# Optimization experiments

Hardware: AMD Instinct MI355X
Metric: run time of the kernel (lower is better)

The kernel has to match this reference:

```python
import jax, jax.numpy as jnp
import numpy as np

HIDDEN = 128; HEADS = 8; HD = HIDDEN // HEADS; NRBF = 50; NLAYERS = 6
CUT = 5.0; MAXZ = 100
N = 5000; E = 100000


def cosine_cutoff(d):
    # cutoff_lower = 0: 0.5*(cos(pi*d/cut)+1) * (d < cut)
    return 0.5 * (jnp.cos(d * (jnp.pi / CUT)) + 1.0) * (d < CUT)


def expnorm_rbf(d, means, betas):
    # ExpNormalSmearing with cutoff_lower=0, alpha = 5/cutoff
    alpha = 5.0 / CUT
    return cosine_cutoff(d)[:, None] * jnp.exp(-betas * (jnp.exp(-alpha * d)[:, None] - means) ** 2)


def layernorm(x, w, b):
    m = x.mean(-1, keepdims=True)
    v = ((x - m) ** 2).mean(-1, keepdims=True)
    return (x - m) / jnp.sqrt(v + 1e-5) * w + b


def setup_inputs():
    key = jax.random.key(0)
    ks = jax.random.split(key, 16)
    start = float(np.exp(-CUT))

    def lin(k, fi, fo):
        return jax.random.normal(k, (fi, fo), jnp.float32) / np.sqrt(fi)

    def lin_l(k, fi, fo):
        return jax.random.normal(k, (NLAYERS, fi, fo), jnp.float32) / np.sqrt(fi)

    return {
        "z": jax.random.randint(ks[0], (N,), 0, MAXZ),
        "edge_index": jax.random.randint(ks[1], (2, E), 0, N),
        "edge_vec": jax.random.normal(ks[2], (E, 3), jnp.float32) * 1.7,
        "emb": jax.random.normal(ks[3], (MAXZ, HIDDEN), jnp.float32),
        "means": jnp.linspace(start, 1.0, NRBF, dtype=jnp.float32),
        "betas": jnp.full((NRBF,), (2.0 / NRBF * (1.0 - start)) ** -2, dtype=jnp.float32),
        "ne_emb": jax.random.normal(ks[4], (MAXZ, HIDDEN), jnp.float32),
        "dpW": lin(ks[5], NRBF, HIDDEN), "dpb": jnp.zeros((HIDDEN,), jnp.float32),
        "cbW": lin(ks[6], 2 * HIDDEN, HIDDEN), "cbb": jnp.zeros((HIDDEN,), jnp.float32),
        "lnw": jnp.ones((NLAYERS, HIDDEN), jnp.float32), "lnb": jnp.zeros((NLAYERS, HIDDEN), jnp.float32),
        "qW": lin_l(ks[7], HIDDEN, HIDDEN), "qb": jnp.zeros((NLAYERS, HIDDEN), jnp.float32),
        "kW": lin_l(ks[8], HIDDEN, HIDDEN), "kb": jnp.zeros((NLAYERS, HIDDEN), jnp.float32),
        "vW": lin_l(ks[9], HIDDEN, 3 * HIDDEN), "vb": jnp.zeros((NLAYERS, 3 * HIDDEN), jnp.float32),
        "oW": lin_l(ks[10], HIDDEN, 3 * HIDDEN), "ob": jnp.zeros((NLAYERS, 3 * HIDDEN), jnp.float32),
        "vecW": lin_l(ks[11], HIDDEN, 3 * HIDDEN),
        "dkW": lin_l(ks[12], NRBF, HIDDEN), "dkb": jnp.zeros((NLAYERS, HIDDEN), jnp.float32),
        "dvW": lin_l(ks[13], NRBF, 3 * HIDDEN), "dvb": jnp.zeros((NLAYERS, 3 * HIDDEN), jnp.float32),
        "onw": jnp.ones((HIDDEN,), jnp.float32), "onb": jnp.zeros((HIDDEN,), jnp.float32),
    }


def _forward(z, edge_index, edge_vec, emb, means, betas, ne_emb, dpW, dpb, cbW, cbb,
             lnw, lnb, qW, qb, kW, kb, vW, vb, oW, ob, vecW, dkW, dkb, dvW, dvb, onw, onb):
    src, dst = edge_index[0], edge_index[1]          # j (source), i (target)
    n = z.shape[0]
    x = emb[z]                                        # [N, H]
    ew = jnp.linalg.norm(edge_vec, axis=1)            # [E]
    ea = expnorm_rbf(ew, means, betas)                # [E, NRBF]
    nonself = src != dst
    # normalize edge vectors except self-loop edges (kept as-is, matching the torch clone/mask)
    evn = edge_vec / jnp.where(nonself, ew, 1.0)[:, None]
    cut_e = cosine_cutoff(ew)                         # [E]

    # --- NeighborEmbedding: self-loops removed from aggregation ---
    W = (ea @ dpW + dpb) * cut_e[:, None]
    W = jnp.where(nonself[:, None], W, 0.0)
    agg = jax.ops.segment_sum(ne_emb[z][src] * W, dst, num_segments=n)
    x = jnp.concatenate([x, agg], axis=1) @ cbW + cbb
    vec = jnp.zeros((n, 3, HIDDEN), x.dtype)

    def layer(carry, p):
        x, vec = carry
        h = layernorm(x, p["lnw"], p["lnb"])
        q = (h @ p["qW"] + p["qb"]).reshape(n, HEADS, HD)
        k = (h @ p["kW"] + p["kb"]).reshape(n, HEADS, HD)
        v = (h @ p["vW"] + p["vb"]).reshape(n, HEADS, 3 * HD)
        vec1, vec2, vec3 = jnp.split(jnp.einsum("nch,hk->nck", vec, p["vecW"]), 3, axis=-1)
        vec_dot = (vec1 * vec2).sum(axis=1)                    # [N, H]
        vec_h = vec.reshape(n, 3, HEADS, HD)
        dk = jax.nn.silu(ea @ p["dkW"] + p["dkb"]).reshape(-1, HEADS, HD)
        dv = jax.nn.silu(ea @ p["dvW"] + p["dvb"]).reshape(-1, HEADS, 3 * HD)
        # per-edge attention weight, silu activation, smoothly cut off
        attn = jax.nn.silu((q[dst] * k[src] * dk).sum(-1)) * cut_e[:, None]   # [E, heads]
        xm, w1, w2 = jnp.split(v[src] * dv, 3, axis=2)                        # each [E, heads, HD]
        xm = xm * attn[:, :, None]
        vecm = vec_h[src] * w1[:, None] + w2[:, None] * evn[:, :, None, None] # [E, 3, heads, HD]
        xa = jax.ops.segment_sum(xm, dst, num_segments=n).reshape(n, HIDDEN)
        va = jax.ops.segment_sum(vecm, dst, num_segments=n).reshape(n, 3, HIDDEN)
        o1, o2, o3 = jnp.split(xa @ p["oW"] + p["ob"], 3, axis=-1)
        dx = vec_dot * o2 + o3
        dvec = vec3 * o1[:, None, :] + va
        return (x + dx, vec + dvec), None

    stacked = {"lnw": lnw, "lnb": lnb, "qW": qW, "qb": qb, "kW": kW, "kb": kb,
               "vW": vW, "vb": vb, "oW": oW, "ob": ob, "vecW": vecW,
               "dkW": dkW, "dkb": dkb, "dvW": dvW, "dvb": dvb}
    (x, vec), _ = jax.lax.scan(layer, (x, vec), stacked)
    x = layernorm(x, onw, onb)
    return x, vec


def reference(z, edge_index, edge_vec, emb, means, betas, ne_emb, dpW, dpb, cbW, cbb,
              lnw, lnb, qW, qb, kW, kb, vW, vb, oW, ob, vecW, dkW, dkb, dvW, dvb, onw, onb):
    return _forward(z, edge_index, edge_vec, emb, means, betas, ne_emb, dpW, dpb, cbW, cbb,
                    lnw, lnb, qW, qb, kW, kb, vW, vb, oW, ob, vecW, dkW, dkb, dvW, dvb, onw, onb)
```

## Files before the change

### kernel.cpp

```cpp
#include <hip/hip_runtime.h>
#include <math.h>

#define HID 128
#define NRBF 50
#define NLAYERS 6
#define CUTV 5.0f
#define KNOTS 1024
#define TSCALE 204.8f
#define TINV   0.0048828125f
#define TROWS  (KNOTS + 1)
#define TRWORDS 512
#define TSTRIDE ((size_t)TROWS * TRWORDS)
#define WCOLS 1408
#define KB 16

typedef unsigned int  uint32;
typedef unsigned short ushort16;
typedef __attribute__((ext_vector_type(8))) short short8;
typedef __attribute__((ext_vector_type(4))) float f32x4;

__device__ __forceinline__ float siluf(float x){ return x / (1.0f + __expf(-x)); }
__device__ __forceinline__ float lerpf(float a, float b, float f){ return fmaf(f, b - a, a); }
__device__ __forceinline__ ushort16 f2b(float x){
    uint32 u = __float_as_uint(x);
    u += 0x7fffu + ((u >> 16) & 1u);
    return (ushort16)(u >> 16);
}
__device__ __forceinline__ float b2f(ushort16 u){ return __uint_as_float(((uint32)u) << 16); }
__device__ __forceinline__ uint32 packp(float a, float b){
    return (uint32)f2b(a) | ((uint32)f2b(b) << 16);
}
__device__ __forceinline__ float plo(uint32 u){ return __uint_as_float(u << 16); }
__device__ __forceinline__ float phi(uint32 u){ return __uint_as_float(u & 0xffff0000u); }
__device__ __forceinline__ float plerp(uint32 u, float f){ float a = plo(u); return fmaf(f, phi(u) - a, a); }

__global__ void k_count(const int* ei, int E, int* counts){
    int e = blockIdx.x*blockDim.x + threadIdx.x;
    if (e < E) atomicAdd(&counts[ei[E + e]], 1);
}

__global__ void k_scan(const int* counts, int* offsets, int* cursor, int n){
    __shared__ int part[1024];
    int tid = threadIdx.x;
    int PER = (n + 1023) >> 10;
    int base = tid * PER;
    int loc[8]; int s = 0;
    #pragma unroll 8
    for (int ii = 0; ii < 8; ii++){
        if (ii < PER){
            int idx = base + ii;
            int c = (idx < n) ? counts[idx] : 0;
            loc[ii] = s; s += c;
        }
    }
    part[tid] = s;
    __syncthreads();
    for (int off = 1; off < 1024; off <<= 1){
        int v = (tid >= off) ? part[tid - off] : 0;
        __syncthreads();
        part[tid] += v;
        __syncthreads();
    }
    int excl = (tid == 0) ? 0 : part[tid - 1];
    #pragma unroll 8
    for (int ii = 0; ii < 8; ii++){
        if (ii < PER){
            int idx = base + ii;
            if (idx < n){ int o = excl + loc[ii]; offsets[idx] = o; cursor[idx] = o; }
        }
    }
    if (tid == 1023) offsets[n] = part[1023];
}

__global__ void k_scatter(const int* ei, int E, int* cursor, int* eperm){
    int e = blockIdx.x*blockDim.x + threadIdx.x;
    if (e < E){
        int d = ei[E + e];
        int pos = atomicAdd(&cursor[d], 1);
        eperm[pos] = e;
    }
}

__global__ __launch_bounds__(256) void k_srcsort(const int* offsets, const int* ei, int* eperm, int N){
    int node = blockIdx.x*4 + (threadIdx.x >> 6);
    int lane = threadIdx.x & 63;
    if (node >= N) return;
    int r0 = offsets[node], r1 = offsets[node+1];
    for (int c0 = r0; c0 < r1; c0 += 64){
        int n = min(64, r1 - c0);
        int e = 0; int key = 0x7fffffff;
        if (lane < n){ e = eperm[c0 + lane]; key = ei[e]; }
        int rank = 0;
        for (int t = 0; t < n; t++){
            int kt = __shfl(key, t, 64);
            if (t != lane && ((kt < key) || (kt == key && t < lane))) rank++;
        }
        if (lane < n) eperm[c0 + rank] = e;
    }
}

__global__ void k_edge_vals(const int* ei, const float* edge_vec, const int* eperm, int E,
                            int4* edata, float4* evn4){
    int row = blockIdx.x*blockDim.x + threadIdx.x;
    if (row >= E) return;
    int e = eperm[row];
    int s = ei[e], d = ei[E + e];
    float vx = edge_vec[e*3+0], vy = edge_vec[e*3+1], vz = edge_vec[e*3+2];
    float ew = sqrtf(vx*vx + vy*vy + vz*vz);
    float cut = (ew < CUTV) ? 0.5f*(__cosf(ew * 0.62831853071795864f) + 1.0f) : 0.0f;
    int ns = (s != d) ? 1 : 0;
    float inv = ns ? (1.0f/ew) : 1.0f;
    float un = fminf(ew * TSCALE, (float)KNOTS);
    int j = (int)un;
    float f = un - (float)j;
    int4 ed; ed.x = s; ed.y = j; ed.z = __float_as_int(f); ed.w = __float_as_int(cut);
    edata[row] = ed;
    float4 ev; ev.x = vx*inv; ev.y = vy*inv; ev.z = vz*inv; ev.w = ns ? 1.0f : 0.0f;
    evn4[row] = ev;
}

__global__ void k_pad(ushort16* hb16, ushort16* vecm, ushort16* xab16, int N, int Nup, int N3up){
    int i = blockIdx.x*blockDim.x + threadIdx.x;
    int hpad = (Nup - N)*HID;
    int vpad = (N3up - 3*N)*HID;
    if (i < hpad){ hb16[(size_t)N*HID + i] = 0; xab16[(size_t)N*HID + i] = 0; }
    if (i < vpad) vecm[(size_t)3*N*HID + i] = 0;
}

__global__ void k_prep_nemb(const int* z, const float* ne_emb, ushort16* nemb16, int total){
    int idx = blockIdx.x*256 + threadIdx.x;
    if (idx >= total) return;
    int n = idx >> 7, h = idx & 127;
    nemb16[idx] = f2b(ne_emb[(size_t)z[n]*HID + h]);
}

__global__ __launch_bounds__(512) void k_build_tables(
    const float* means, const float* betas,
    const float* dkW, const float* dkb, const float* dvW, const float* dvb,
    uint32* Tp){
    int jb = blockIdx.x * KB;
    int l  = blockIdx.y;
    int c  = threadIdx.x;
    __shared__ float ea_s[KB+1][NRBF+2];
    for (int idx = c; idx < (KB+1)*NRBF; idx += 512){
        int kk = idx / NRBF, r = idx - kk*NRBF;
        float d = (jb + kk) * TINV;
        float cut = (d < CUTV) ? 0.5f*(__cosf(d * 0.62831853071795864f) + 1.0f) : 0.0f;
        float u = __expf(-d) - means[r];
        ea_s[kk][r] = cut * __expf(-betas[r]*u*u);
    }
    __syncthreads();
    int h = c >> 2, i = c & 3;
    const float* Wcol; int stride; float bias;
    if (i == 0){
        Wcol = dkW + (size_t)l*NRBF*HID + h; stride = HID;
        bias = dkb[(size_t)l*HID + h];
    } else {
        int col = ((h >> 4)*48 + (h & 15)) + 16*(i-1);
        Wcol = dvW + (size_t)l*NRBF*384 + col; stride = 384;
        bias = dvb[(size_t)l*384 + col];
    }
    float a[KB+1];
    #pragma unroll
    for (int k = 0; k <= KB; k++) a[k] = bias;
    for (int r = 0; r < NRBF; r++){
        float w = Wcol[(size_t)r*stride];
        #pragma unroll
        for (int k = 0; k <= KB; k++) a[k] += ea_s[k][r]*w;
    }
    uint32* dst = Tp + (size_t)l*TSTRIDE + (size_t)jb*TRWORDS + c;
    float sp = siluf(a[0]);
    #pragma unroll
    for (int k = 0; k < KB; k++){
        int j = jb + k;
        if (j >= TROWS) break;
        float sn = siluf(a[k+1]);
        dst[(size_t)k*TRWORDS] = packp(sp, sn);
        sp = sn;
    }
}

__global__ __launch_bounds__(128) void k_build_ne(
    const float* means, const float* betas,
    const float* dpW, const float* dpb, uint32* Tne32){
    int j = blockIdx.x, c = threadIdx.x;
    __shared__ float ea0[NRBF], ea1[NRBF];
    float d0 = j * TINV, d1 = (j+1) * TINV;
    float c0 = (d0 < CUTV) ? 0.5f*(__cosf(d0 * 0.62831853071795864f) + 1.0f) : 0.0f;
    float c1 = (d1 < CUTV) ? 0.5f*(__cosf(d1 * 0.62831853071795864f) + 1.0f) : 0.0f;
    if (c < NRBF){
        float m = means[c], be = betas[c];
        float u0 = __expf(-d0) - m, u1 = __expf(-d1) - m;
        ea0[c] = c0 * __expf(-be*u0*u0);
        ea1[c] = c1 * __expf(-be*u1*u1);
    }
    __syncthreads();
    float a0 = dpb[c], a1 = a0;
    #pragma unroll
    for (int r = 0; r < NRBF; r++){ float w = dpW[r*HID + c]; a0 += ea0[r]*w; a1 += ea1[r]*w; }
    Tne32[(size_t)j*HID + c] = packp(a0*c0, a1*c1);
}

__global__ __launch_bounds__(256) void k_build_wt(
    const float* qW, const float* kW, const float* vW, const float* vecW, const float* oW,
    ushort16* WT){
    int l = blockIdx.y; int c0 = blockIdx.x*32;
    __shared__ ushort16 t[128][33];
    for (int i = threadIdx.x; i < 128*32; i += 256){
        int k = i >> 5, c = i & 31;
        int gcol = c0 + c;
        const float* W; int C; int oc;
        if (gcol < 128)      { W = qW   + (size_t)l*HID*128; C = 128; oc = gcol; }
        else if (gcol < 640) {
            int s = gcol - 128; int h = s >> 2, si = s & 3;
            if (si == 3){ W = kW + (size_t)l*HID*128; C = 128; oc = h; }
            else        { W = vW + (size_t)l*HID*384; C = 384; oc = (h>>4)*48 + (h&15) + 16*si; }
        }
        else if (gcol < 1024){ W = vecW + (size_t)l*HID*384; C = 384; oc = gcol-640; }
        else                 { W = oW   + (size_t)l*HID*384; C = 384; oc = gcol-1024; }
        t[k][c] = f2b(W[(size_t)k*C + oc]);
    }
    __syncthreads();
    ushort16* dst = WT + (size_t)l*WCOLS*HID + (size_t)c0*HID;
    for (int i = threadIdx.x; i < 128*32; i += 256){
        int c = i >> 7, k = i & 127;
        dst[(size_t)c*HID + k] = t[k][c];
    }
}

__global__ __launch_bounds__(512) void k_build_bias(
    const float* kb, const float* vb, float* kvbias){
    int l = blockIdx.x, s = threadIdx.x;
    int h = s >> 2, i = s & 3;
    float v = (i == 3) ? kb[(size_t)l*HID + h]
                       : vb[(size_t)l*384 + (h>>4)*48 + (h&15) + 16*i];
    kvbias[(size_t)l*512 + s] = v;
}

__global__ __launch_bounds__(256) void k_mfma01(
    const ushort16* __restrict__ hb16, const ushort16* __restrict__ vecm,
    const ushort16* __restrict__ WT, const float* __restrict__ qbias,
    const float* __restrict__ kvbias,
    float* __restrict__ qo, ushort16* __restrict__ vpack,
    ushort16* __restrict__ vecout, int N){
    int NT1 = (N + 63) >> 6;
    int NT3 = (3*N + 63) >> 6;
    int b = blockIdx.x;
    int cg, rblk;
    if (b < 10*NT1){ cg = b / NT1; rblk = (b - cg*NT1)*64; }
    else { int b2 = b - 10*NT1; int c2 = b2 / NT3; cg = 10 + c2; rblk = (b2 - c2*NT3)*64; }
    const ushort16* A; int R; int cblk; const ushort16* wt;
    if (cg < 10){ A = hb16; R = N;   cblk = cg*64;      wt = WT; }
    else        { A = vecm; R = 3*N; cblk = (cg-10)*64; wt = WT + (size_t)640*HID; }
    int wave = threadIdx.x >> 6, lane = threadIdx.x & 63;
    int r0 = rblk + wave*16;
    int l16 = lane & 15, lg = lane >> 4;
    short8 a[4];
    const ushort16* ar = A + (size_t)(r0 + l16)*HID + lg*8;
    #pragma unroll
    for (int ks = 0; ks < 4; ks++) a[ks] = *(const short8*)(ar + ks*32);
    f32x4 acc[4];
    #pragma unroll
    for (int ct = 0; ct < 4; ct++){ acc[ct][0]=0.f; acc[ct][1]=0.f; acc[ct][2]=0.f; acc[ct][3]=0.f; }
    #pragma unroll
    for (int ct = 0; ct < 4; ct++){
        const ushort16* br = wt + (size_t)(cblk + ct*16 + l16)*HID + lg*8;
        #pragma unroll
        for (int ks = 0; ks < 4; ks++){
            short8 bfr = *(const short8*)(br + ks*32);
            acc[ct] = __builtin_amdgcn_mfma_f32_16x16x32_bf16(a[ks], bfr, acc[ct], 0, 0, 0);
        }
    }
    __shared__ ushort16 lds[64][72];
    if (cg < 2){
        #pragma unroll
        for (int ct = 0; ct < 4; ct++){
            int gc = cblk + ct*16 + l16;
            float bb = qbias[gc];
            #pragma unroll
            for (int rg = 0; rg < 4; rg++){
                int row = r0 + lg*4 + rg;
                if (row < R) qo[(size_t)row*HID + gc] = acc[ct][rg] + bb;
            }
        }
        return;
    }
    const float* bias = (cg < 10) ? (kvbias + (cblk - 128)) : nullptr;
    #pragma unroll
    for (int ct = 0; ct < 4; ct++){
        int lc = ct*16 + l16;
        float bb = bias ? bias[lc] : 0.f;
        #pragma unroll
        for (int rg = 0; rg < 4; rg++)
            lds[wave*16 + lg*4 + rg][lc] = f2b(acc[ct][rg] + bb);
    }
    __syncthreads();
    ushort16* out; int stride, colbase;
    if (cg < 10){ out = vpack;  stride = 512; colbase = cblk - 128; }
    else        { out = vecout; stride = 384; colbase = cblk; }
    const uint32* l32 = (const uint32*)&lds[0][0];
    #pragma unroll
    for (int it = 0; it < 8; it++){
        int idx = it*256 + threadIdx.x;
        int row = idx >> 5, cp = idx & 31;
        int grow = rblk + row;
        if (grow < R){
            uint32 val = l32[row*36 + cp];
            *((uint32*)(out + (size_t)grow*stride + colbase) + cp) = val;
        }
    }
}

__global__ __launch_bounds__(128) void k_ne_agg(
    const int* __restrict__ offsets, const int4* __restrict__ edata,
    const uint32* __restrict__ Tne32, const ushort16* __restrict__ nemb16,
    float* __restrict__ agg){
    int i = blockIdx.x, h = threadIdx.x;
    float acc = 0.f;
    int r0 = offsets[i], r1 = offsets[i+1];
    for (int t0 = r0; t0 < r1; t0 += 4){
        uint32 tn_[4]; ushort16 nb_[4]; float f_[4]; int s_[4];
        #pragma unroll
        for (int u = 0; u < 4; u++){
            int row = min(t0 + u, r1 - 1);
            int4 ed = edata[row];
            s_[u] = ed.x;
            f_[u] = __int_as_float(ed.z);
            tn_[u] = Tne32[(size_t)ed.y*HID + h];
            nb_[u] = nemb16[(size_t)ed.x*HID + h];
        }
        #pragma unroll
        for (int u = 0; u < 4; u++){
            if (t0 + u >= r1) break;
            if (s_[u] != i) acc += plerp(tn_[u], f_[u]) * b2f(nb_[u]);
        }
    }
    agg[(size_t)i*HID + h] = acc;
}

__global__ __launch_bounds__(128) void k_combine_ln(
    const int* z, const float* emb, const float* agg, const float* cbW, const float* cbb,
    const float* lnw0, const float* lnb0,
    float* x, ushort16* hb16, float* vec, ushort16* vecm, uint32* vecpack, int N){
    int n0 = blockIdx.x*8, h = threadIdx.x;
    __shared__ float in_s[8][2*HID];
    int nr = min(8, N - n0);
    for (int m = 0; m < nr; m++){
        in_s[m][h]       = emb[(size_t)z[n0+m]*HID + h];
        in_s[m][HID + h] = agg[(size_t)(n0+m)*HID + h];
    }
    __syncthreads();
    float acc[8];
    #pragma unroll
    for (int m = 0; m < 8; m++) acc[m] = 0.f;
    for (int kk = 0; kk < 2*HID; kk += 4){
        float w0 = cbW[(kk+0)*HID + h], w1 = cbW[(kk+1)*HID + h];
        float w2 = cbW[(kk+2)*HID + h], w3 = cbW[(kk+3)*HID + h];
        #pragma unroll
        for (int m = 0; m < 8; m++){
            const float* a = &in_s[m][kk];
            acc[m] += a[0]*w0 + a[1]*w1 + a[2]*w2 + a[3]*w3;
        }
    }
    float bias = cbb[h], w = lnw0[h], bb = lnb0[h];
    __shared__ float r1_[2], r2_[2];
    int wid = h >> 6;
    for (int m = 0; m < nr; m++){
        int n = n0 + m;
        float v = acc[m] + bias;
        x[(size_t)n*HID + h] = v;
        float s1 = v, s2 = v*v;
        #pragma unroll
        for (int o = 32; o; o >>= 1){ s1 += __shfl_xor(s1, o, 64); s2 += __shfl_xor(s2, o, 64); }
        if ((h & 63) == 0){ r1_[wid] = s1; r2_[wid] = s2; }
        __syncthreads();
        float sum = r1_[0] + r1_[1], sumsq = r2_[0] + r2_[1];
        float mean = sum * (1.f/HID);
        float var = sumsq * (1.f/HID) - mean*mean;
        float inv = rsqrtf(var + 1e-5f);
        hb16[(size_t)n*HID + h] = f2b((v - mean)*inv*w + bb);
        __syncthreads();
        vec [(size_t)n*384 + h]       = 0.f;
        vec [(size_t)n*384 + 128 + h] = 0.f;
        vec [(size_t)n*384 + 256 + h] = 0.f;
        vecm[(size_t)n*384 + h]       = 0;
        vecm[(size_t)n*384 + 128 + h] = 0;
        vecm[(size_t)n*384 + 256 + h] = 0;
        vecpack[(size_t)n*256 + 2*h]     = 0;
        vecpack[(size_t)n*256 + 2*h + 1] = 0;
    }
}

__global__ __launch_bounds__(128) void k_edge_agg(
    const int* __restrict__ offsets, const int4* __restrict__ edata,
    const float4* __restrict__ evn4, const uint32* __restrict__ Tp,
    const float* __restrict__ q, const ushort16* __restrict__ vpack,
    const uint32* __restrict__ vecpack,
    ushort16* __restrict__ xa16, float* __restrict__ va){
    int i = blockIdx.x, h = threadIdx.x;
    float qv = q[(size_t)i*HID + h];
    float axa = 0.f, av0 = 0.f, av1 = 0.f, av2 = 0.f;
    int r0 = offsets[i], r1 = offsets[i+1];
    for (int t0 = r0; t0 < r1; t0 += 4){
        float f_[4], cut_[4], ex_[4], ey_[4], ez_[4];
        uint4 t4_[4];
        uint2 vp_[4], vc_[4];
        #pragma unroll
        for (int u = 0; u < 4; u++){
            int row = min(t0 + u, r1 - 1);
            int4 ed = edata[row];
            int s = ed.x, j = ed.y;
            f_[u]   = __int_as_float(ed.z);
            cut_[u] = __int_as_float(ed.w);
            t4_[u] = *(const uint4*)(Tp + (size_t)j*TRWORDS + 4*h);
            vp_[u] = *(const uint2*)((const uint32*)(vpack + (size_t)s*512) + 2*h);
            vc_[u] = *(const uint2*)(vecpack + (size_t)s*256 + 2*h);
            float4 ev = evn4[row];
            ex_[u] = ev.x; ey_[u] = ev.y; ez_[u] = ev.z;
        }
        #pragma unroll
        for (int u = 0; u < 4; u++){
            if (t0 + u >= r1) break;
            float f = f_[u];
            float dk = plerp(t4_[u].x, f);
            float kv = phi(vp_[u].y);
            float p = qv * kv * dk;
            p += __shfl_xor(p, 1, 64);
            p += __shfl_xor(p, 2, 64);
            p += __shfl_xor(p, 4, 64);
            p += __shfl_xor(p, 8, 64);
            float attn = siluf(p) * cut_[u];
            float dv0 = plerp(t4_[u].y, f);
            float dv1 = plerp(t4_[u].z, f);
            float dv2 = plerp(t4_[u].w, f);
            axa += plo(vp_[u].x) * dv0 * attn;
            float w1v = phi(vp_[u].x) * dv1;
            float w2v = plo(vp_[u].y) * dv2;
            av0 += plo(vc_[u].x)*w1v + w2v*ex_[u];
            av1 += phi(vc_[u].x)*w1v + w2v*ey_[u];
            av2 += plo(vc_[u].y)*w1v + w2v*ez_[u];
        }
    }
    xa16[(size_t)i*HID + h] = f2b(axa);
    va[(size_t)i*384 + h]       = av0;
    va[(size_t)i*384 + 128 + h] = av1;
    va[(size_t)i*384 + 256 + h] = av2;
}

#define OROWS 32
__global__ __launch_bounds__(256) void k_oupd(
    const ushort16* __restrict__ xab16, const ushort16* __restrict__ WT,
    const float* __restrict__ obias,
    float* __restrict__ x, float* __restrict__ vec, ushort16* __restrict__ vecm,
    uint32* __restrict__ vecpack,
    const ushort16* __restrict__ vecout, const float* __restrict__ va,
    const float* __restrict__ lnw_n, const float* __restrict__ lnb_n,
    ushort16* __restrict__ hb16, float* __restrict__ outx, float* __restrict__ outv,
    int N, int fin){
    __shared__ float o_s[OROWS][385];
    int tile = blockIdx.x; int r0 = tile*OROWS;
    int wid = threadIdx.x >> 6, lane = threadIdx.x & 63;
    int l16 = lane & 15, lg = lane >> 4;
    {
        int rr = r0 + (wid & 1)*16;
        const ushort16* ar = xab16 + (size_t)(rr + l16)*HID + lg*8;
        short8 a[4];
        #pragma unroll
        for (int ks = 0; ks < 4; ks++) a[ks] = *(const short8*)(ar + ks*32);
        int cbase = (wid >> 1)*192;
        const ushort16* wt = WT + (size_t)1024*HID;
        #pragma unroll
        for (int ct = 0; ct < 12; ct++){
            f32x4 acc; acc[0]=0.f; acc[1]=0.f; acc[2]=0.f; acc[3]=0.f;
            const ushort16* br = wt + (size_t)(cbase + ct*16 + l16)*HID + lg*8;
            #pragma unroll
            for (int ks = 0; ks < 4; ks++){
                short8 b = *(const short8*)(br + ks*32);
                acc = __builtin_amdgcn_mfma_f32_16x16x32_bf16(a[ks], b, acc, 0, 0, 0);
            }
            int gc = cbase + ct*16 + l16;
            float bb = obias[gc];
            #pragma unroll
            for (int rg = 0; rg < 4; rg++)
                o_s[(wid & 1)*16 + lg*4 + rg][gc] = acc[rg] + bb;
        }
    }
    __syncthreads();
    for (int pass = 0; pass < 8; pass++){
        int nrow = pass*4 + wid;
        int n = r0 + nrow;
        if (n >= N) break;
        const ushort16* vo = vecout + (size_t)n*1152;
        const float* o_r = o_s[nrow];
        size_t vb = (size_t)n*384;
        float xva, xvb, v0a, v0b, v1a, v1b, v2a, v2b;
        #pragma unroll
        for (int half = 0; half < 2; half++){
            int hh = lane + half*64;
            float vdot = b2f(vo[hh])*b2f(vo[128+hh]) + b2f(vo[384+hh])*b2f(vo[512+hh])
                       + b2f(vo[768+hh])*b2f(vo[896+hh]);
            float o1 = o_r[hh], o2 = o_r[128+hh], o3 = o_r[256+hh];
            float xv = x[(size_t)n*HID + hh] + vdot*o2 + o3;
            float v0 = vec[vb + hh]       + b2f(vo[256  + hh])*o1 + va[vb + hh];
            float v1 = vec[vb + 128 + hh] + b2f(vo[640  + hh])*o1 + va[vb + 128 + hh];
            float v2 = vec[vb + 256 + hh] + b2f(vo[1024 + hh])*o1 + va[vb + 256 + hh];
            if (half == 0){ xva = xv; v0a = v0; v1a = v1; v2a = v2; }
            else          { xvb = xv; v0b = v0; v1b = v1; v2b = v2; }
        }
        float s1 = xva + xvb, s2 = xva*xva + xvb*xvb;
        #pragma unroll
        for (int o = 32; o; o >>= 1){ s1 += __shfl_xor(s1, o, 64); s2 += __shfl_xor(s2, o, 64); }
        float mean = s1 * (1.f/HID);
        float var = s2 * (1.f/HID) - mean*mean;
        float inv = rsqrtf(var + 1e-5f);
        #pragma unroll
        for (int half = 0; half < 2; half++){
            int hh = lane + half*64;
            float xv = half ? xvb : xva;
            float v0 = half ? v0b : v0a;
            float v1 = half ? v1b : v1a;
            float v2 = half ? v2b : v2a;
            float lnv = (xv - mean)*inv*lnw_n[hh] + lnb_n[hh];
            if (!fin){
                x[(size_t)n*HID + hh] = xv;
                vec[vb + hh] = v0; vec[vb + 128 + hh] = v1; vec[vb + 256 + hh] = v2;
                vecm[vb + hh] = f2b(v0); vecm[vb + 128 + hh] = f2b(v1); vecm[vb + 256 + hh] = f2b(v2);
                vecpack[(size_t)n*256 + 2*hh]     = packp(v0, v1);
                vecpack[(size_t)n*256 + 2*hh + 1] = packp(v2, 0.f);
                hb16[(size_t)n*HID + hh] = f2b(lnv);
            } else {
                outx[(size_t)n*HID + hh] = lnv;
                outv[vb + hh] = v0; outv[vb + 128 + hh] = v1; outv[vb + 256 + hh] = v2;
            }
        }
    }
}

extern "C" void kernel_launch(void* const* d_in, const int* in_sizes, int n_in,
                              void* d_out, int out_size, void* d_ws, size_t ws_size,
                              hipStream_t stream){
    const int*   z        = (const int*)  d_in[0];
    const int*   ei       = (const int*)  d_in[1];
    const float* edge_vec = (const float*)d_in[2];
    const float* emb      = (const float*)d_in[3];
    const float* means    = (const float*)d_in[4];
    const float* betas    = (const float*)d_in[5];
    const float* ne_emb   = (const float*)d_in[6];
    const float* dpW      = (const float*)d_in[7];
    const float* dpb      = (const float*)d_in[8];
    const float* cbW      = (const float*)d_in[9];
    const float* cbb      = (const float*)d_in[10];
    const float* lnw      = (const float*)d_in[11];
    const float* lnb      = (const float*)d_in[12];
    const float* qW       = (const float*)d_in[13];
    const float* qb       = (const float*)d_in[14];
    const float* kW       = (const float*)d_in[15];
    const float* kb       = (const float*)d_in[16];
    const float* vW       = (const float*)d_in[17];
    const float* vb       = (const float*)d_in[18];
    const float* oW       = (const float*)d_in[19];
    const float* obias    = (const float*)d_in[20];
    const float* vecW     = (const float*)d_in[21];
    const float* dkW      = (const float*)d_in[22];
    const float* dkb      = (const float*)d_in[23];
    const float* dvW      = (const float*)d_in[24];
    const float* dvb      = (const float*)d_in[25];
    const float* onw      = (const float*)d_in[26];
    const float* onb      = (const float*)d_in[27];

    int N = in_sizes[0];
    int E = in_sizes[1] / 2;
    int Nup  = ((N + 63) >> 6) << 6;
    int N3up = ((3*N + 63) >> 6) << 6;

    char* p = (char*)d_ws;
    auto alloc = [&](size_t bytes){ void* r = (void*)p; p += (bytes + 255) & ~(size_t)255; return r; };
    int*      counts  = (int*)     alloc((size_t)N*4);
    int*      offsets = (int*)     alloc((size_t)(N+1)*4);
    int*      cursor  = (int*)     alloc((size_t)N*4);
    int*      eperm   = (int*)     alloc((size_t)E*4);
    int4*     edata   = (int4*)    alloc((size_t)E*16);
    float4*   evn4    = (float4*)  alloc((size_t)E*16);
    uint32*   Tp      = (uint32*)  alloc((size_t)NLAYERS*TSTRIDE*4);
    uint32*   Tne32   = (uint32*)  alloc((size_t)TROWS*HID*4);
    ushort16* WT      = (ushort16*)alloc((size_t)NLAYERS*WCOLS*HID*2);
    float*    kvbias  = (float*)   alloc((size_t)NLAYERS*512*4);
    ushort16* nemb16  = (ushort16*)alloc((size_t)N*HID*2);
    float*    agg     = (float*)   alloc((size_t)N*HID*4);
    float*    xb      = (float*)   alloc((size_t)N*HID*4);
    ushort16* hb16    = (ushort16*)alloc((size_t)Nup*HID*2);
    float*    qb_     = (float*)   alloc((size_t)N*HID*4);
    ushort16* vpack   = (ushort16*)alloc((size_t)N*512*2);
    uint32*   vecpack = (uint32*)  alloc((size_t)N*256*4);
    ushort16* vecm    = (ushort16*)alloc((size_t)N3up*HID*2);
    float*    vecb    = (float*)   alloc((size_t)N*384*4);
    ushort16* vecout  = (ushort16*)alloc((size_t)N*1152*2);
    ushort16* xab16   = (ushort16*)alloc((size_t)Nup*HID*2);
    float*    vab     = (float*)   alloc((size_t)N*384*4);

    hipMemsetAsync(counts, 0, (size_t)N*4, stream);
    k_count<<<(E+255)/256, 256, 0, stream>>>(ei, E, counts);
    k_scan<<<1, 1024, 0, stream>>>(counts, offsets, cursor, N);
    k_scatter<<<(E+255)/256, 256, 0, stream>>>(ei, E, cursor, eperm);
    k_srcsort<<<(N+3)/4, 256, 0, stream>>>(offsets, ei, eperm, N);
    k_edge_vals<<<(E+255)/256, 256, 0, stream>>>(ei, edge_vec, eperm, E, edata, evn4);
    k_pad<<<((Nup-N)*HID + (N3up-3*N)*HID + 255)/256 + 1, 256, 0, stream>>>(hb16, vecm, xab16, N, Nup, N3up);
    k_prep_nemb<<<(N*HID+255)/256, 256, 0, stream>>>(z, ne_emb, nemb16, N*HID);

    k_build_tables<<<dim3((TROWS + KB - 1)/KB, NLAYERS), 512, 0, stream>>>(means, betas, dkW, dkb, dvW, dvb, Tp);
    k_build_ne<<<TROWS, 128, 0, stream>>>(means, betas, dpW, dpb, Tne32);
    k_build_wt<<<dim3(WCOLS/32, NLAYERS), 256, 0, stream>>>(qW, kW, vW, vecW, oW, WT);
    k_build_bias<<<NLAYERS, 512, 0, stream>>>(kb, vb, kvbias);
    k_ne_agg<<<N, 128, 0, stream>>>(offsets, edata, Tne32, nemb16, agg);
    k_combine_ln<<<(N+7)/8, 128, 0, stream>>>(z, emb, agg, cbW, cbb, lnw, lnb,
                                              xb, hb16, vecb, vecm, vecpack, N);

    float* outx = (float*)d_out;
    float* outv = (float*)d_out + (size_t)N*HID;

    int NT1 = (N + 63) >> 6;
    int NT3 = (3*N + 63) >> 6;
    for (int l = 0; l < NLAYERS; l++){
        const ushort16* WTl = WT + (size_t)l*WCOLS*HID;
        k_mfma01<<<10*NT1 + 6*NT3, 256, 0, stream>>>(hb16, vecm, WTl,
            qb + (size_t)l*HID, kvbias + (size_t)l*512,
            qb_, vpack, vecout, N);
        k_edge_agg<<<N, 128, 0, stream>>>(offsets, edata, evn4, Tp + (size_t)l*TSTRIDE,
                                          qb_, vpack, vecpack, xab16, vab);
        int fin = (l == NLAYERS-1);
        k_oupd<<<(N + OROWS - 1)/OROWS, 256, 0, stream>>>(xab16, WTl, obias + (size_t)l*384,
            xb, vecb, vecm, vecpack, vecout, vab,
            fin ? onw : lnw + (size_t)(l+1)*HID,
            fin ? onb : lnb + (size_t)(l+1)*HID,
            hb16, outx, outv, N, fin);
    }
}
```

Measured before the change: 615.2 us.

## Merge setup kernels into one launch, fuse srcsort with edge values, two nodes per edge_agg block

Eight independent preprocessing kernels (count, nemb conversion, padding, table builds, weight transpose, bias pack) are folded into a single block-dispatched k_setup launch. The source-sort kernel now also computes the per-edge data directly, which removes the separate k_edge_vals pass and its re-read of eperm. k_edge_agg now processes two nodes per 256-thread block instead of one node per 128-thread block. The aim is to cut launch overhead and serial dependencies in setup. The cost is a heterogeneous mega-kernel where the table-build blocks now run 256 threads looping twice, so they may become the tail.

```diff
diff --git a/kernel.cpp b/kernel.cpp
--- a/kernel.cpp
+++ b/kernel.cpp
@@ -13,6 +13,10 @@
 #define TSTRIDE ((size_t)TROWS * TRWORDS)
 #define WCOLS 1408
 #define KB 16
+#define TBLK ((TROWS + KB - 1)/KB)
+#define TB   (TBLK*NLAYERS)
+#define NEB  ((TROWS + 1)/2)
+#define WTB  ((WCOLS/32)*NLAYERS)
 
 typedef unsigned int  uint32;
 typedef unsigned short ushort16;
@@ -33,10 +37,159 @@
 __device__ __forceinline__ float plo(uint32 u){ return __uint_as_float(u << 16); }
 __device__ __forceinline__ float phi(uint32 u){ return __uint_as_float(u & 0xffff0000u); }
 __device__ __forceinline__ float plerp(uint32 u, float f){ float a = plo(u); return fmaf(f, phi(u) - a, a); }
-
-__global__ void k_count(const int* ei, int E, int* counts){
-    int e = blockIdx.x*blockDim.x + threadIdx.x;
-    if (e < E) atomicAdd(&counts[ei[E + e]], 1);
+__device__ __forceinline__ float cutoff(float d){
+    return (d < CUTV) ? 0.5f*(__cosf(d * 0.62831853071795864f) + 1.0f) : 0.0f;
+}
+
+__global__ __launch_bounds__(256) void k_setup(
+    const int* __restrict__ ei, int E, int* __restrict__ counts,
+    const int* __restrict__ z, const float* __restrict__ ne_emb, ushort16* __restrict__ nemb16, int N,
+    ushort16* __restrict__ hb16, ushort16* __restrict__ vecm, ushort16* __restrict__ xab16, int Nup, int N3up,
+    const float* __restrict__ means, const float* __restrict__ betas,
+    const float* __restrict__ dkW, const float* __restrict__ dkb,
+    const float* __restrict__ dvW, const float* __restrict__ dvb, uint32* __restrict__ Tp,
+    const float* __restrict__ dpW, const float* __restrict__ dpb, uint32* __restrict__ Tne32,
+    const float* __restrict__ qW, const float* __restrict__ kW, const float* __restrict__ vW,
+    const float* __restrict__ vecW, const float* __restrict__ oW, ushort16* __restrict__ WT,
+    const float* __restrict__ kb, const float* __restrict__ vb, float* __restrict__ kvbias){
+    __shared__ float ea_s[KB+1][NRBF+2];
+    __shared__ float ne0[2][NRBF], ne1[2][NRBF];
+    __shared__ ushort16 tws[128][33];
+    int tid = threadIdx.x;
+    int CB  = (E + 255) >> 8;
+    int NPB = (N*HID + 255) >> 8;
+    int b = blockIdx.x;
+    if (b < CB){
+        int e = b*256 + tid;
+        if (e < E) atomicAdd(&counts[ei[E + e]], 1);
+        return;
+    }
+    b -= CB;
+    if (b < NPB){
+        int idx = b*256 + tid;
+        if (idx < N*HID){
+            int n = idx >> 7, h = idx & 127;
+            nemb16[idx] = f2b(ne_emb[(size_t)z[n]*HID + h]);
+        }
+        return;
+    }
+    b -= NPB;
+    if (b < 64){
+        int i = b*256 + tid;
+        int hpad = (Nup - N)*HID;
+        int vpad = (N3up - 3*N)*HID;
+        if (i < hpad){ hb16[(size_t)N*HID + i] = 0; xab16[(size_t)N*HID + i] = 0; }
+        if (i < vpad) vecm[(size_t)3*N*HID + i] = 0;
+        return;
+    }
+    b -= 64;
+    if (b < TB){
+        int jb = (b % TBLK) * KB;
+        int l  = b / TBLK;
+        for (int idx = tid; idx < (KB+1)*NRBF; idx += 256){
+            int kk = idx / NRBF, r = idx - kk*NRBF;
+            float d = (jb + kk) * TINV;
+            float u = __expf(-d) - means[r];
+            ea_s[kk][r] = cutoff(d) * __expf(-betas[r]*u*u);
+        }
+        __syncthreads();
+        #pragma unroll
+        for (int half = 0; half < 2; half++){
+            int c = tid + half*256;
+            int h = c >> 2, i = c & 3;
+            const float* Wcol; int stride; float bias;
+            if (i == 0){
+                Wcol = dkW + (size_t)l*NRBF*HID + h; stride = HID;
+                bias = dkb[(size_t)l*HID + h];
+            } else {
+                int col = ((h >> 4)*48 + (h & 15)) + 16*(i-1);
+                Wcol = dvW + (size_t)l*NRBF*384 + col; stride = 384;
+                bias = dvb[(size_t)l*384 + col];
+            }
+            float a[KB+1];
+            #pragma unroll
+            for (int k = 0; k <= KB; k++) a[k] = bias;
+            for (int r = 0; r < NRBF; r++){
+                float w = Wcol[(size_t)r*stride];
+                #pragma unroll
+                for (int k = 0; k <= KB; k++) a[k] += ea_s[k][r]*w;
+            }
+            uint32* dst = Tp + (size_t)l*TSTRIDE + (size_t)jb*TRWORDS + c;
+            float sp = siluf(a[0]);
+            #pragma unroll
+            for (int k = 0; k < KB; k++){
+                int j = jb + k;
+                if (j >= TROWS) break;
+                float sn = siluf(a[k+1]);
+                dst[(size_t)k*TRWORDS] = packp(sp, sn);
+                sp = sn;
+            }
+        }
+        return;
+    }
+    b -= TB;
+    if (b < NEB){
+        int half = tid >> 7, c = tid & 127;
+        int j = b*2 + half;
+        bool ok = (j < TROWS);
+        if (ok && c < NRBF){
+            float d0 = j * TINV, d1 = (j+1) * TINV;
+            float m = means[c], be = betas[c];
+            float u0 = __expf(-d0) - m, u1 = __expf(-d1) - m;
+            ne0[half][c] = cutoff(d0) * __expf(-be*u0*u0);
+            ne1[half][c] = cutoff(d1) * __expf(-be*u1*u1);
+        }
+        __syncthreads();
+        if (ok){
+            float c0 = cutoff(j * TINV), c1 = cutoff((j+1) * TINV);
+            float a0 = dpb[c], a1 = a0;
+            #pragma unroll
+            for (int r = 0; r < NRBF; r++){
+                float w = dpW[r*HID + c];
+                a0 += ne0[half][r]*w; a1 += ne1[half][r]*w;
+            }
+            Tne32[(size_t)j*HID + c] = packp(a0*c0, a1*c1);
+        }
+        return;
+    }
+    b -= NEB;
+    if (b < WTB){
+        int l = b / (WCOLS/32);
+        int c0 = (b % (WCOLS/32))*32;
+        for (int i = tid; i < 128*32; i += 256){
+            int k = i >> 5, c = i & 31;
+            int gcol = c0 + c;
+            const float* W; int C; int oc;
+            if (gcol < 128)      { W = qW   + (size_t)l*HID*128; C = 128; oc = gcol; }
+            else if (gcol < 640) {
+                int s = gcol - 128; int h = s >> 2, si = s & 3;
+                if (si == 3){ W = kW + (size_t)l*HID*128; C = 128; oc = h; }
+                else        { W = vW + (size_t)l*HID*384; C = 384; oc = (h>>4)*48 + (h&15) + 16*si; }
+            }
+            else if (gcol < 1024){ W = vecW + (size_t)l*HID*384; C = 384; oc = gcol-640; }
+            else                 { W = oW   + (size_t)l*HID*384; C = 384; oc = gcol-1024; }
+            tws[k][c] = f2b(W[(size_t)k*C + oc]);
+        }
+        __syncthreads();
+        ushort16* dst = WT + (size_t)l*WCOLS*HID + (size_t)c0*HID;
+        for (int i = tid; i < 128*32; i += 256){
+            int c = i >> 7, k = i & 127;
+            dst[(size_t)c*HID + k] = tws[k][c];
+        }
+        return;
+    }
+    b -= WTB;
+    {
+        int l = b;
+        #pragma unroll
+        for (int half = 0; half < 2; half++){
+            int s = tid + half*256;
+            int h = s >> 2, i = s & 3;
+            float v = (i == 3) ? kb[(size_t)l*HID + h]
+                               : vb[(size_t)l*384 + (h>>4)*48 + (h&15) + 16*i];
+            kvbias[(size_t)l*512 + s] = v;
+        }
+    }
 }
 
 __global__ void k_scan(const int* counts, int* offsets, int* cursor, int n){
@@ -81,7 +234,9 @@
     }
 }
 
-__global__ __launch_bounds__(256) void k_srcsort(const int* offsets, const int* ei, int* eperm, int N){
+__global__ __launch_bounds__(256) void k_srcsort_vals(
+    const int* offsets, const int* ei, const int* eperm, const float* edge_vec, int N,
+    int4* edata, float4* evn4){
     int node = blockIdx.x*4 + (threadIdx.x >> 6);
     int lane = threadIdx.x & 63;
     if (node >= N) return;
@@ -95,146 +250,23 @@
             int kt = __shfl(key, t, 64);
             if (t != lane && ((kt < key) || (kt == key && t < lane))) rank++;
         }
-        if (lane < n) eperm[c0 + rank] = e;
-    }
-}
-
-__global__ void k_edge_vals(const int* ei, const float* edge_vec, const int* eperm, int E,
-                            int4* edata, float4* evn4){
-    int row = blockIdx.x*blockDim.x + threadIdx.x;
-    if (row >= E) return;
-    int e = eperm[row];
-    int s = ei[e], d = ei[E + e];
-    float vx = edge_vec[e*3+0], vy = edge_vec[e*3+1], vz = edge_vec[e*3+2];
-    float ew = sqrtf(vx*vx + vy*vy + vz*vz);
-    float cut = (ew < CUTV) ? 0.5f*(__cosf(ew * 0.62831853071795864f) + 1.0f) : 0.0f;
-    int ns = (s != d) ? 1 : 0;
-    float inv = ns ? (1.0f/ew) : 1.0f;
-    float un = fminf(ew * TSCALE, (float)KNOTS);
-    int j = (int)un;
-    float f = un - (float)j;
-    int4 ed; ed.x = s; ed.y = j; ed.z = __float_as_int(f); ed.w = __float_as_int(cut);
-    edata[row] = ed;
-    float4 ev; ev.x = vx*inv; ev.y = vy*inv; ev.z = vz*inv; ev.w = ns ? 1.0f : 0.0f;
-    evn4[row] = ev;
-}
-
-__global__ void k_pad(ushort16* hb16, ushort16* vecm, ushort16* xab16, int N, int Nup, int N3up){
-    int i = blockIdx.x*blockDim.x + threadIdx.x;
-    int hpad = (Nup - N)*HID;
-    int vpad = (N3up - 3*N)*HID;
-    if (i < hpad){ hb16[(size_t)N*HID + i] = 0; xab16[(size_t)N*HID + i] = 0; }
-    if (i < vpad) vecm[(size_t)3*N*HID + i] = 0;
-}
-
-__global__ void k_prep_nemb(const int* z, const float* ne_emb, ushort16* nemb16, int total){
-    int idx = blockIdx.x*256 + threadIdx.x;
-    if (idx >= total) return;
-    int n = idx >> 7, h = idx & 127;
-    nemb16[idx] = f2b(ne_emb[(size_t)z[n]*HID + h]);
-}
-
-__global__ __launch_bounds__(512) void k_build_tables(
-    const float* means, const float* betas,
-    const float* dkW, const float* dkb, const float* dvW, const float* dvb,
-    uint32* Tp){
-    int jb = blockIdx.x * KB;
-    int l  = blockIdx.y;
-    int c  = threadIdx.x;
-    __shared__ float ea_s[KB+1][NRBF+2];
-    for (int idx = c; idx < (KB+1)*NRBF; idx += 512){
-        int kk = idx / NRBF, r = idx - kk*NRBF;
-        float d = (jb + kk) * TINV;
-        float cut = (d < CUTV) ? 0.5f*(__cosf(d * 0.62831853071795864f) + 1.0f) : 0.0f;
-        float u = __expf(-d) - means[r];
-        ea_s[kk][r] = cut * __expf(-betas[r]*u*u);
-    }
-    __syncthreads();
-    int h = c >> 2, i = c & 3;
-    const float* Wcol; int stride; float bias;
-    if (i == 0){
-        Wcol = dkW + (size_t)l*NRBF*HID + h; stride = HID;
-        bias = dkb[(size_t)l*HID + h];
-    } else {
-        int col = ((h >> 4)*48 + (h & 15)) + 16*(i-1);
-        Wcol = dvW + (size_t)l*NRBF*384 + col; stride = 384;
-        bias = dvb[(size_t)l*384 + col];
-    }
-    float a[KB+1];
-    #pragma unroll
-    for (int k = 0; k <= KB; k++) a[k] = bias;
-    for (int r = 0; r < NRBF; r++){
-        float w = Wcol[(size_t)r*stride];
-        #pragma unroll
-        for (int k = 0; k <= KB; k++) a[k] += ea_s[k][r]*w;
-    }
-    uint32* dst = Tp + (size_t)l*TSTRIDE + (size_t)jb*TRWORDS + c;
-    float sp = siluf(a[0]);
-    #pragma unroll
-    for (int k = 0; k < KB; k++){
-        int j = jb + k;
-        if (j >= TROWS) break;
-        float sn = siluf(a[k+1]);
-        dst[(size_t)k*TRWORDS] = packp(sp, sn);
-        sp = sn;
-    }
-}
-
-__global__ __launch_bounds__(128) void k_build_ne(
-    const float* means, const float* betas,
-    const float* dpW, const float* dpb, uint32* Tne32){
-    int j = blockIdx.x, c = threadIdx.x;
-    __shared__ float ea0[NRBF], ea1[NRBF];
-    float d0 = j * TINV, d1 = (j+1) * TINV;
-    float c0 = (d0 < CUTV) ? 0.5f*(__cosf(d0 * 0.62831853071795864f) + 1.0f) : 0.0f;
-    float c1 = (d1 < CUTV) ? 0.5f*(__cosf(d1 * 0.62831853071795864f) + 1.0f) : 0.0f;
-    if (c < NRBF){
-        float m = means[c], be = betas[c];
-        float u0 = __expf(-d0) - m, u1 = __expf(-d1) - m;
-        ea0[c] = c0 * __expf(-be*u0*u0);
-        ea1[c] = c1 * __expf(-be*u1*u1);
-    }
-    __syncthreads();
-    float a0 = dpb[c], a1 = a0;
-    #pragma unroll
-    for (int r = 0; r < NRBF; r++){ float w = dpW[r*HID + c]; a0 += ea0[r]*w; a1 += ea1[r]*w; }
-    Tne32[(size_t)j*HID + c] = packp(a0*c0, a1*c1);
-}
-
-__global__ __launch_bounds__(256) void k_build_wt(
-    const float* qW, const float* kW, const float* vW, const float* vecW, const float* oW,
-    ushort16* WT){
-    int l = blockIdx.y; int c0 = blockIdx.x*32;
-    __shared__ ushort16 t[128][33];
-    for (int i = threadIdx.x; i < 128*32; i += 256){
-        int k = i >> 5, c = i & 31;
-        int gcol = c0 + c;
-        const float* W; int C; int oc;
-        if (gcol < 128)      { W = qW   + (size_t)l*HID*128; C = 128; oc = gcol; }
-        else if (gcol < 640) {
-            int s = gcol - 128; int h = s >> 2, si = s & 3;
-            if (si == 3){ W = kW + (size_t)l*HID*128; C = 128; oc = h; }
-            else        { W = vW + (size_t)l*HID*384; C = 384; oc = (h>>4)*48 + (h&15) + 16*si; }
-        }
-        else if (gcol < 1024){ W = vecW + (size_t)l*HID*384; C = 384; oc = gcol-640; }
-        else                 { W = oW   + (size_t)l*HID*384; C = 384; oc = gcol-1024; }
-        t[k][c] = f2b(W[(size_t)k*C + oc]);
-    }
-    __syncthreads();
-    ushort16* dst = WT + (size_t)l*WCOLS*HID + (size_t)c0*HID;
-    for (int i = threadIdx.x; i < 128*32; i += 256){
-        int c = i >> 7, k = i & 127;
-        dst[(size_t)c*HID + k] = t[k][c];
-    }
-}
-
-__global__ __launch_bounds__(512) void k_build_bias(
-    const float* kb, const float* vb, float* kvbias){
-    int l = blockIdx.x, s = threadIdx.x;
-    int h = s >> 2, i = s & 3;
-    float v = (i == 3) ? kb[(size_t)l*HID + h]
-                       : vb[(size_t)l*384 + (h>>4)*48 + (h&15) + 16*i];
-    kvbias[(size_t)l*512 + s] = v;
+        if (lane < n){
+            int s = key;
+            float vx = edge_vec[e*3+0], vy = edge_vec[e*3+1], vz = edge_vec[e*3+2];
+            float ew = sqrtf(vx*vx + vy*vy + vz*vz);
+            float cut = cutoff(ew);
+            int ns = (s != node) ? 1 : 0;
+            float inv = ns ? (1.0f/ew) : 1.0f;
+            float un = fminf(ew * TSCALE, (float)KNOTS);
+            int j = (int)un;
+            float f = un - (float)j;
+            int row = c0 + rank;
+            int4 ed; ed.x = s; ed.y = j; ed.z = __float_as_int(f); ed.w = __float_as_int(cut);
+            edata[row] = ed;
+            float4 ev; ev.x = vx*inv; ev.y = vy*inv; ev.z = vz*inv; ev.w = ns ? 1.0f : 0.0f;
+            evn4[row] = ev;
+        }
+    }
 }
 
 __global__ __launch_bounds__(256) void k_mfma01(
@@ -391,13 +423,15 @@
     }
 }
 
-__global__ __launch_bounds__(128) void k_edge_agg(
+__global__ __launch_bounds__(256) void k_edge_agg(
     const int* __restrict__ offsets, const int4* __restrict__ edata,
     const float4* __restrict__ evn4, const uint32* __restrict__ Tp,
     const float* __restrict__ q, const ushort16* __restrict__ vpack,
     const uint32* __restrict__ vecpack,
-    ushort16* __restrict__ xa16, float* __restrict__ va){
-    int i = blockIdx.x, h = threadIdx.x;
+    ushort16* __restrict__ xa16, float* __restrict__ va, int N){
+    int i = blockIdx.x*2 + (threadIdx.x >> 7);
+    int h = threadIdx.x & 127;
+    if (i >= N) return;
     float qv = q[(size_t)i*HID + h];
     float axa = 0.f, av0 = 0.f, av1 = 0.f, av2 = 0.f;
     int r0 = offsets[i], r1 = offsets[i+1];
@@ -599,18 +633,21 @@
     float*    vab     = (float*)   alloc((size_t)N*384*4);
 
     hipMemsetAsync(counts, 0, (size_t)N*4, stream);
-    k_count<<<(E+255)/256, 256, 0, stream>>>(ei, E, counts);
+
+    int CB  = (E + 255) >> 8;
+    int NPB = (N*HID + 255) >> 8;
+    int setup_blocks = CB + NPB + 64 + TB + NEB + WTB + NLAYERS;
+    k_setup<<<setup_blocks, 256, 0, stream>>>(
+        ei, E, counts,
+        z, ne_emb, nemb16, N,
+        hb16, vecm, xab16, Nup, N3up,
+        means, betas, dkW, dkb, dvW, dvb, Tp,
+        dpW, dpb, Tne32,
+        qW, kW, vW, vecW, oW, WT,
+        kb, vb, kvbias);
     k_scan<<<1, 1024, 0, stream>>>(counts, offsets, cursor, N);
     k_scatter<<<(E+255)/256, 256, 0, stream>>>(ei, E, cursor, eperm);
-    k_srcsort<<<(N+3)/4, 256, 0, stream>>>(offsets, ei, eperm, N);
-    k_edge_vals<<<(E+255)/256, 256, 0, stream>>>(ei, edge_vec, eperm, E, edata, evn4);
-    k_pad<<<((Nup-N)*HID + (N3up-3*N)*HID + 255)/256 + 1, 256, 0, stream>>>(hb16, vecm, xab16, N, Nup, N3up);
-    k_prep_nemb<<<(N*HID+255)/256, 256, 0, stream>>>(z, ne_emb, nemb16, N*HID);
-
-    k_build_tables<<<dim3((TROWS + KB - 1)/KB, NLAYERS), 512, 0, stream>>>(means, betas, dkW, dkb, dvW, dvb, Tp);
-    k_build_ne<<<TROWS, 128, 0, stream>>>(means, betas, dpW, dpb, Tne32);
-    k_build_wt<<<dim3(WCOLS/32, NLAYERS), 256, 0, stream>>>(qW, kW, vW, vecW, oW, WT);
-    k_build_bias<<<NLAYERS, 512, 0, stream>>>(kb, vb, kvbias);
+    k_srcsort_vals<<<(N+3)/4, 256, 0, stream>>>(offsets, ei, eperm, edge_vec, N, edata, evn4);
     k_ne_agg<<<N, 128, 0, stream>>>(offsets, edata, Tne32, nemb16, agg);
     k_combine_ln<<<(N+7)/8, 128, 0, stream>>>(z, emb, agg, cbW, cbb, lnw, lnb,
                                               xb, hb16, vecb, vecm, vecpack, N);
@@ -625,8 +662,8 @@
         k_mfma01<<<10*NT1 + 6*NT3, 256, 0, stream>>>(hb16, vecm, WTl,
             qb + (size_t)l*HID, kvbias + (size_t)l*512,
             qb_, vpack, vecout, N);
-        k_edge_agg<<<N, 128, 0, stream>>>(offsets, edata, evn4, Tp + (size_t)l*TSTRIDE,
-                                          qb_, vpack, vecpack, xab16, vab);
+        k_edge_agg<<<(N+1)/2, 256, 0, stream>>>(offsets, edata, evn4, Tp + (size_t)l*TSTRIDE,
+                                                qb_, vpack, vecpack, xab16, vab, N);
         int fin = (l == NLAYERS-1);
         k_oupd<<<(N + OROWS - 1)/OROWS, 256, 0, stream>>>(xab16, WTl, obias + (size_t)l*384,
             xb, vecb, vecm, vecpack, vecout, vab,
```

After: 698.8 us. +13.6%, slower.
